# Kernel tuning notes

Hardware: AMD Instinct MI355X
Metric: run time of the kernel (lower is better)

## Reference

```python
import jax, jax.numpy as jnp
import numpy as np

N_NODES = 100000
N_EDGES = 640000
D_IN = 128
D_OUT = 128


def setup_inputs() -> dict:
    key = jax.random.key(0)
    k_x, k_w, k_v, k_r, k_c = jax.random.split(key, 5)
    x = jax.random.normal(k_x, (N_NODES, D_IN), dtype=jnp.float32)
    # Xavier-uniform init for weights, zeros for bias (matches module init)
    limit = float(np.sqrt(6.0 / (D_IN + D_OUT)))
    weights = jax.random.uniform(k_w, (D_IN, D_OUT), dtype=jnp.float32,
                                 minval=-limit, maxval=limit)
    bias = jnp.zeros((D_OUT,), dtype=jnp.float32)
    # Sparse normalized adjacency in COO form: value[e] * y[col[e]] scattered to row[e]
    edge_val = jax.random.uniform(k_v, (N_EDGES,), dtype=jnp.float32)
    row = jax.random.randint(k_r, (N_EDGES,), 0, N_NODES, dtype=jnp.int32)
    col = jax.random.randint(k_c, (N_EDGES,), 0, N_NODES, dtype=jnp.int32)
    return {"x": x, "weights": weights, "bias": bias,
            "edge_val": edge_val, "row": row, "col": col}


def reference(x, weights, bias, edge_val, row, col):
    # y = x @ W  (dense GEMM)  [N, D_OUT]
    y = x @ weights
    # SpMM: out[i] = sum_{e: row[e]==i} edge_val[e] * y[col[e]]
    msg = edge_val[:, None] * y[col]            # [E, D_OUT] irregular gather
    agg = jax.ops.segment_sum(msg, row, num_segments=x.shape[0])
    return agg + bias
```

## Files before the change

### kernel.cpp

```cpp
#include <hip/hip_runtime.h>
#include <hip/hip_bf16.h>


#define N_NODES 100000
#define N_EDGES 640000
#define D 128
#define ELL_K 16
#define OVF_CAP 8192
#define NB 391
#define BCAP 2048
#define CHUNK 4096
#define NCHUNKS 157

typedef __attribute__((ext_vector_type(8))) short short8;
typedef __attribute__((ext_vector_type(4))) float f32x4;
typedef __attribute__((ext_vector_type(4))) ushort us4;

__device__ __forceinline__ ushort f2bf(float f) {
    uint u = __float_as_uint(f);
    u += 0x7fff + ((u >> 16) & 1);
    return (ushort)(u >> 16);
}
__device__ __forceinline__ float bflo(uint u) { return __uint_as_float(u << 16); }
__device__ __forceinline__ float bfhi(uint u) { return __uint_as_float(u & 0xffff0000u); }

__global__ __launch_bounds__(256, 2) void gemm_xw(const float* __restrict__ x,
                                                  const float* __restrict__ w,
                                                  ushort* __restrict__ y,
                                                  int* __restrict__ bucketCursor,
                                                  int* __restrict__ ovfCnt) {
    __shared__ ushort wt[128 * 128];
    const int tid = threadIdx.x;

    int gz = blockIdx.x * 256 + tid;
    if (gz < NB) bucketCursor[gz] = gz * BCAP;
    if (gz == 0) *ovfCnt = 0;

    #pragma unroll
    for (int it = 0; it < 16; ++it) {
        int idx4 = tid + it * 256;
        int k = idx4 >> 5;
        int n0 = (idx4 & 31) * 4;
        float4 v = *(const float4*)(w + (size_t)idx4 * 4);
        float vv[4] = {v.x, v.y, v.z, v.w};
        #pragma unroll
        for (int q = 0; q < 4; ++q) {
            int n = n0 + q;
            wt[n * 128 + (k ^ ((n & 7) << 3))] = f2bf(vv[q]);
        }
    }
    __syncthreads();

    const int lane = tid & 63;
    const int l15 = lane & 15;
    const int h = lane >> 4;

    short8 bfr[8][4];
    #pragma unroll
    for (int j = 0; j < 8; ++j) {
        int n = 16 * j + l15;
        #pragma unroll
        for (int ks = 0; ks < 4; ++ks) {
            int k0 = 32 * ks + 8 * h;
            bfr[j][ks] = *(const short8*)&wt[n * 128 + (k0 ^ ((n & 7) << 3))];
        }
    }

    const int waveGlobal = blockIdx.x * 4 + (tid >> 6);
    const int nWaves = gridDim.x * 4;
    const int nTiles = N_NODES / 16;

    for (int t = waveGlobal; t < nTiles; t += nWaves) {
        const float* xr = x + (size_t)(t * 16 + l15) * D;
        float4 xb[8];
        #pragma unroll
        for (int ks = 0; ks < 4; ++ks) {
            xb[2 * ks]     = *(const float4*)(xr + 32 * ks + 8 * h);
            xb[2 * ks + 1] = *(const float4*)(xr + 32 * ks + 8 * h + 4);
        }
        f32x4 acc[8];
        #pragma unroll
        for (int j = 0; j < 8; ++j) acc[j] = (f32x4){0.f, 0.f, 0.f, 0.f};
        #pragma unroll
        for (int ks = 0; ks < 4; ++ks) {
            const float* p0 = (const float*)&xb[2 * ks];
            const float* p1 = (const float*)&xb[2 * ks + 1];
            short8 a;
            a[0] = f2bf(p0[0]); a[1] = f2bf(p0[1]); a[2] = f2bf(p0[2]); a[3] = f2bf(p0[3]);
            a[4] = f2bf(p1[0]); a[5] = f2bf(p1[1]); a[6] = f2bf(p1[2]); a[7] = f2bf(p1[3]);
            #pragma unroll
            for (int j = 0; j < 8; ++j)
                acc[j] = __builtin_amdgcn_mfma_f32_16x16x32_bf16(bfr[j][ks], a, acc[j], 0, 0, 0);
        }
        ushort* yn = y + (size_t)(t * 16 + l15) * D;
        #pragma unroll
        for (int j = 0; j < 8; ++j) {
            us4 o;
            o.x = f2bf(acc[j][0]); o.y = f2bf(acc[j][1]);
            o.z = f2bf(acc[j][2]); o.w = f2bf(acc[j][3]);
            *(us4*)(yn + 16 * j + 4 * h) = o;
        }
    }
}

__global__ __launch_bounds__(256) void partition_edges(const float* __restrict__ ev,
                                                       const int* __restrict__ row,
                                                       const int* __restrict__ col,
                                                       int* __restrict__ bucketCursor,
                                                       uint2* __restrict__ es0,
                                                       int* __restrict__ ovfCnt,
                                                       int* __restrict__ ovfRow,
                                                       int* __restrict__ ovfCol,
                                                       float* __restrict__ ovfVal) {
    __shared__ int hist[NB];
    __shared__ int cur[NB];
    const int tid = threadIdx.x;
    const int base = blockIdx.x * CHUNK;

    for (int t = tid; t < NB; t += 256) hist[t] = 0;
    __syncthreads();

    #pragma unroll
    for (int it = 0; it < CHUNK / 256; ++it) {
        int i = base + it * 256 + tid;
        if (i < N_EDGES) atomicAdd(&hist[row[i] >> 8], 1);
    }
    __syncthreads();

    for (int t = tid; t < NB; t += 256) {
        int hcnt = hist[t];
        cur[t] = (hcnt > 0) ? atomicAdd(&bucketCursor[t], hcnt) : 0;
    }
    __syncthreads();

    #pragma unroll
    for (int it = 0; it < CHUNK / 256; ++it) {
        int i = base + it * 256 + tid;
        if (i < N_EDGES) {
            int r = row[i];
            int b = r >> 8;
            int p = atomicAdd(&cur[b], 1);
            if (p < (b + 1) * BCAP) {
                uint2 e;
                e.x = __float_as_uint(ev[i]);
                e.y = (uint)col[i] | ((uint)(r & 255) << 20);
                es0[p] = e;
            } else {
                int q = atomicAdd(ovfCnt, 1);
                if (q < OVF_CAP) {
                    ovfRow[q] = r;
                    ovfCol[q] = col[i];
                    ovfVal[q] = ev[i];
                }
            }
        }
    }
}

__global__ __launch_bounds__(256) void build_ell(const uint2* __restrict__ es0,
                                                 const int* __restrict__ bucketCursor,
                                                 float2* __restrict__ es,
                                                 int* __restrict__ counts,
                                                 int* __restrict__ ovfCnt,
                                                 int* __restrict__ ovfRow,
                                                 int* __restrict__ ovfCol,
                                                 float* __restrict__ ovfVal) {
    __shared__ float2 ell[256 * ELL_K];
    __shared__ int lcnt[256];
    const int tid = threadIdx.x;
    const int b = blockIdx.x;

    lcnt[tid] = 0;
    __syncthreads();

    int cnt = bucketCursor[b] - b * BCAP;
    if (cnt > BCAP) cnt = BCAP;
    const uint2* src = es0 + (size_t)b * BCAP;

    for (int i = tid; i < cnt; i += 256) {
        uint2 e = src[i];
        int r = e.y >> 20;
        int p = atomicAdd(&lcnt[r], 1);
        if (p < ELL_K) {
            float2 rec;
            rec.x = __uint_as_float(e.x);
            rec.y = __uint_as_float(e.y & 0xFFFFFu);
            ell[r * ELL_K + p] = rec;
        } else {
            int q = atomicAdd(ovfCnt, 1);
            if (q < OVF_CAP) {
                ovfRow[q] = b * 256 + r;
                ovfCol[q] = (int)(e.y & 0xFFFFFu);
                ovfVal[q] = __uint_as_float(e.x);
            }
        }
    }
    __syncthreads();

    const int nbase = b * 256;
    int nvalid = N_NODES - nbase;
    if (nvalid > 256) nvalid = 256;

    if (tid < nvalid) counts[nbase + tid] = lcnt[tid];

    float4* dst4 = (float4*)(es + (size_t)nbase * ELL_K);
    const float4* ell4 = (const float4*)ell;
    for (int t = tid; t < nvalid * (ELL_K / 2); t += 256)
        dst4[t] = ell4[t];
}

__global__ __launch_bounds__(256) void spmm_ell(const ushort* __restrict__ y,
                                                const float2* __restrict__ es,
                                                const int* __restrict__ counts,
                                                const float* __restrict__ bias,
                                                float* __restrict__ out) {
    const int tid = threadIdx.x;
    const int lane = tid & 63;
    const int wid = blockIdx.x * 4 + (tid >> 6);
    const float2 b2 = *(const float2*)(bias + lane * 2);

    #pragma unroll 1
    for (int rep = 0; rep < 2; ++rep) {
        const int n = __builtin_amdgcn_readfirstlane(wid * 2 + rep);
        int deg = counts[n];
        if (deg > ELL_K) deg = ELL_K;
        const float4* er = (const float4*)(es + (size_t)n * ELL_K);

        float ax = 0.f, ay = 0.f;
        #pragma unroll
        for (int g = 0; g < 4; ++g) {
            if (4 * g < deg) {
                float4 sA = er[2 * g];
                float4 sB = er[2 * g + 1];
                int c0 = __float_as_int(sA.y);
                int c1 = (4 * g + 1 < deg) ? __float_as_int(sA.w) : c0;
                int c2 = (4 * g + 2 < deg) ? __float_as_int(sB.y) : c0;
                int c3 = (4 * g + 3 < deg) ? __float_as_int(sB.w) : c0;
                uint u0 = *(const uint*)(y + ((size_t)c0 << 7) + lane * 2);
                uint u1 = *(const uint*)(y + ((size_t)c1 << 7) + lane * 2);
                uint u2 = *(const uint*)(y + ((size_t)c2 << 7) + lane * 2);
                uint u3 = *(const uint*)(y + ((size_t)c3 << 7) + lane * 2);
                float v0 = sA.x;
                float v1 = (4 * g + 1 < deg) ? sA.z : 0.f;
                float v2 = (4 * g + 2 < deg) ? sB.x : 0.f;
                float v3 = (4 * g + 3 < deg) ? sB.z : 0.f;
                ax += v0 * bflo(u0); ay += v0 * bfhi(u0);
                ax += v1 * bflo(u1); ay += v1 * bfhi(u1);
                ax += v2 * bflo(u2); ay += v2 * bfhi(u2);
                ax += v3 * bflo(u3); ay += v3 * bfhi(u3);
            }
        }
        float2 o = {ax + b2.x, ay + b2.y};
        *(float2*)(out + ((size_t)n << 7) + lane * 2) = o;
    }
}

__global__ void ovf_fix(const ushort* __restrict__ y, const int* __restrict__ ovfRow,
                        const int* __restrict__ ovfCol, const float* __restrict__ ovfVal,
                        const int* __restrict__ ovfCnt, float* __restrict__ out) {
    int nOvf = *ovfCnt;
    if (nOvf > OVF_CAP) nOvf = OVF_CAP;
    int total = nOvf * 32;
    for (int idx = blockIdx.x * 256 + threadIdx.x; idx < total; idx += gridDim.x * 256) {
        int e = idx >> 5;
        int c = idx & 31;
        int r = ovfRow[e];
        int col = ovfCol[e];
        float v = ovfVal[e];
        uint2 u = *(const uint2*)(y + ((size_t)col << 7) + c * 4);
        atomicAdd(&out[(size_t)r * D + c * 4 + 0], v * bflo(u.x));
        atomicAdd(&out[(size_t)r * D + c * 4 + 1], v * bfhi(u.x));
        atomicAdd(&out[(size_t)r * D + c * 4 + 2], v * bflo(u.y));
        atomicAdd(&out[(size_t)r * D + c * 4 + 3], v * bfhi(u.y));
    }
}

extern "C" void kernel_launch(void* const* d_in, const int* in_sizes, int n_in,
                              void* d_out, int out_size, void* d_ws, size_t ws_size,
                              hipStream_t stream) {
    const float* x = (const float*)d_in[0];
    const float* w = (const float*)d_in[1];
    const float* bias = (const float*)d_in[2];
    const float* ev = (const float*)d_in[3];
    const int* row = (const int*)d_in[4];
    const int* col = (const int*)d_in[5];
    float* out = (float*)d_out;

    size_t off = 0;
    auto carve = [&](size_t bytes) -> void* {
        void* p = (char*)d_ws + off;
        off += (bytes + 255) & ~(size_t)255;
        return p;
    };
    ushort* y = (ushort*)carve((size_t)N_NODES * D * sizeof(ushort));
    int* counts = (int*)carve((size_t)N_NODES * sizeof(int));
    float2* es = (float2*)carve((size_t)N_NODES * ELL_K * sizeof(float2));
    uint2* es0 = (uint2*)carve((size_t)NB * BCAP * sizeof(uint2));
    int* bucketCursor = (int*)carve(NB * sizeof(int));
    int* ovfCnt = (int*)carve(sizeof(int));
    int* ovfRow = (int*)carve(OVF_CAP * sizeof(int));
    int* ovfCol = (int*)carve(OVF_CAP * sizeof(int));
    float* ovfVal = (float*)carve(OVF_CAP * sizeof(float));

    gemm_xw<<<512, 256, 0, stream>>>(x, w, y, bucketCursor, ovfCnt);
    partition_edges<<<NCHUNKS, 256, 0, stream>>>(ev, row, col, bucketCursor, es0,
                                                 ovfCnt, ovfRow, ovfCol, ovfVal);
    build_ell<<<NB, 256, 0, stream>>>(es0, bucketCursor, es, counts,
                                      ovfCnt, ovfRow, ovfCol, ovfVal);
    spmm_ell<<<N_NODES / 8, 256, 0, stream>>>(y, es, counts, bias, out);
    ovf_fix<<<16, 256, 0, stream>>>(y, ovfRow, ovfCol, ovfVal, ovfCnt, out);
}
```

Baseline: 85.75 us.

## Fuse GEMM with edge partitioning and widen SpMM gathers to 16-byte loads

Merges the dense GEMM and the edge-partition pass into one launch. The first blocks bucket edges while the remaining blocks compute tiles of the GEMM, so the two independent stages can run concurrently and one launch is removed. Cursor initialisation moves to a memset and bucket counts are now kept relative to each bucket. In the SpMM, each wave now handles four nodes per step with 16 lanes per row and uint4 loads, which widens the gather accesses. This adds more registers per lane, and the memset adds a small extra operation to the stream.

```diff
diff --git a/kernel.cpp b/kernel.cpp
--- a/kernel.cpp
+++ b/kernel.cpp
@@ -11,6 +11,8 @@
 #define BCAP 2048
 #define CHUNK 4096
 #define NCHUNKS 157
+#define GEMM_BLOCKS 782
+#define N_TILES 6250
 
 typedef __attribute__((ext_vector_type(8))) short short8;
 typedef __attribute__((ext_vector_type(4))) float f32x4;
@@ -24,17 +26,69 @@
 __device__ __forceinline__ float bflo(uint u) { return __uint_as_float(u << 16); }
 __device__ __forceinline__ float bfhi(uint u) { return __uint_as_float(u & 0xffff0000u); }
 
-__global__ __launch_bounds__(256, 2) void gemm_xw(const float* __restrict__ x,
-                                                  const float* __restrict__ w,
-                                                  ushort* __restrict__ y,
-                                                  int* __restrict__ bucketCursor,
-                                                  int* __restrict__ ovfCnt) {
-    __shared__ ushort wt[128 * 128];
+__global__ __launch_bounds__(256, 2) void gemm_partition(const float* __restrict__ x,
+                                                         const float* __restrict__ w,
+                                                         ushort* __restrict__ y,
+                                                         const float* __restrict__ ev,
+                                                         const int* __restrict__ row,
+                                                         const int* __restrict__ col,
+                                                         int* __restrict__ bucketCnt,
+                                                         uint2* __restrict__ es0,
+                                                         int* __restrict__ ovfCnt,
+                                                         int* __restrict__ ovfRow,
+                                                         int* __restrict__ ovfCol,
+                                                         float* __restrict__ ovfVal) {
+    __shared__ union {
+        ushort wt[128 * 128];
+        struct { int hist[NB]; int cur[NB]; } p;
+    } sm;
     const int tid = threadIdx.x;
 
-    int gz = blockIdx.x * 256 + tid;
-    if (gz < NB) bucketCursor[gz] = gz * BCAP;
-    if (gz == 0) *ovfCnt = 0;
+    if (blockIdx.x < NCHUNKS) {
+        const int base = blockIdx.x * CHUNK;
+        for (int t = tid; t < NB; t += 256) sm.p.hist[t] = 0;
+        __syncthreads();
+
+        #pragma unroll
+        for (int it = 0; it < CHUNK / 256; ++it) {
+            int i = base + it * 256 + tid;
+            if (i < N_EDGES) atomicAdd(&sm.p.hist[row[i] >> 8], 1);
+        }
+        __syncthreads();
+
+        for (int t = tid; t < NB; t += 256) {
+            int h = sm.p.hist[t];
+            int start = (h > 0) ? atomicAdd(&bucketCnt[t], h) : 0;
+            sm.p.cur[t] = t * BCAP + start;
+        }
+        __syncthreads();
+
+        #pragma unroll
+        for (int it = 0; it < CHUNK / 256; ++it) {
+            int i = base + it * 256 + tid;
+            if (i < N_EDGES) {
+                int r = row[i];
+                int b = r >> 8;
+                int p = atomicAdd(&sm.p.cur[b], 1);
+                if (p < (b + 1) * BCAP) {
+                    uint2 e;
+                    e.x = __float_as_uint(ev[i]);
+                    e.y = (uint)col[i] | ((uint)(r & 255) << 20);
+                    es0[p] = e;
+                } else {
+                    int q = atomicAdd(ovfCnt, 1);
+                    if (q < OVF_CAP) {
+                        ovfRow[q] = r;
+                        ovfCol[q] = col[i];
+                        ovfVal[q] = ev[i];
+                    }
+                }
+            }
+        }
+        return;
+    }
+
+    const int bid = blockIdx.x - NCHUNKS;
 
     #pragma unroll
     for (int it = 0; it < 16; ++it) {
@@ -46,7 +100,7 @@
         #pragma unroll
         for (int q = 0; q < 4; ++q) {
             int n = n0 + q;
-            wt[n * 128 + (k ^ ((n & 7) << 3))] = f2bf(vv[q]);
+            sm.wt[n * 128 + (k ^ ((n & 7) << 3))] = f2bf(vv[q]);
         }
     }
     __syncthreads();
@@ -62,15 +116,15 @@
         #pragma unroll
         for (int ks = 0; ks < 4; ++ks) {
             int k0 = 32 * ks + 8 * h;
-            bfr[j][ks] = *(const short8*)&wt[n * 128 + (k0 ^ ((n & 7) << 3))];
-        }
-    }
-
-    const int waveGlobal = blockIdx.x * 4 + (tid >> 6);
-    const int nWaves = gridDim.x * 4;
-    const int nTiles = N_NODES / 16;
-
-    for (int t = waveGlobal; t < nTiles; t += nWaves) {
+            bfr[j][ks] = *(const short8*)&sm.wt[n * 128 + (k0 ^ ((n & 7) << 3))];
+        }
+    }
+
+    const int t0 = bid * 8 + (tid >> 6) * 2;
+    #pragma unroll 1
+    for (int rep = 0; rep < 2; ++rep) {
+        int t = t0 + rep;
+        if (t >= N_TILES) continue;
         const float* xr = x + (size_t)(t * 16 + l15) * D;
         float4 xb[8];
         #pragma unroll
@@ -103,62 +157,8 @@
     }
 }
 
-__global__ __launch_bounds__(256) void partition_edges(const float* __restrict__ ev,
-                                                       const int* __restrict__ row,
-                                                       const int* __restrict__ col,
-                                                       int* __restrict__ bucketCursor,
-                                                       uint2* __restrict__ es0,
-                                                       int* __restrict__ ovfCnt,
-                                                       int* __restrict__ ovfRow,
-                                                       int* __restrict__ ovfCol,
-                                                       float* __restrict__ ovfVal) {
-    __shared__ int hist[NB];
-    __shared__ int cur[NB];
-    const int tid = threadIdx.x;
-    const int base = blockIdx.x * CHUNK;
-
-    for (int t = tid; t < NB; t += 256) hist[t] = 0;
-    __syncthreads();
-
-    #pragma unroll
-    for (int it = 0; it < CHUNK / 256; ++it) {
-        int i = base + it * 256 + tid;
-        if (i < N_EDGES) atomicAdd(&hist[row[i] >> 8], 1);
-    }
-    __syncthreads();
-
-    for (int t = tid; t < NB; t += 256) {
-        int hcnt = hist[t];
-        cur[t] = (hcnt > 0) ? atomicAdd(&bucketCursor[t], hcnt) : 0;
-    }
-    __syncthreads();
-
-    #pragma unroll
-    for (int it = 0; it < CHUNK / 256; ++it) {
-        int i = base + it * 256 + tid;
-        if (i < N_EDGES) {
-            int r = row[i];
-            int b = r >> 8;
-            int p = atomicAdd(&cur[b], 1);
-            if (p < (b + 1) * BCAP) {
-                uint2 e;
-                e.x = __float_as_uint(ev[i]);
-                e.y = (uint)col[i] | ((uint)(r & 255) << 20);
-                es0[p] = e;
-            } else {
-                int q = atomicAdd(ovfCnt, 1);
-                if (q < OVF_CAP) {
-                    ovfRow[q] = r;
-                    ovfCol[q] = col[i];
-                    ovfVal[q] = ev[i];
-                }
-            }
-        }
-    }
-}
-
 __global__ __launch_bounds__(256) void build_ell(const uint2* __restrict__ es0,
-                                                 const int* __restrict__ bucketCursor,
+                                                 const int* __restrict__ bucketCnt,
                                                  float2* __restrict__ es,
                                                  int* __restrict__ counts,
                                                  int* __restrict__ ovfCnt,
@@ -173,7 +173,7 @@
     lcnt[tid] = 0;
     __syncthreads();
 
-    int cnt = bucketCursor[b] - b * BCAP;
+    int cnt = bucketCnt[b];
     if (cnt > BCAP) cnt = BCAP;
     const uint2* src = es0 + (size_t)b * BCAP;
 
@@ -216,17 +216,23 @@
                                                 float* __restrict__ out) {
     const int tid = threadIdx.x;
     const int lane = tid & 63;
+    const int c16 = lane & 15;
+    const int sub = lane >> 4;
     const int wid = blockIdx.x * 4 + (tid >> 6);
-    const float2 b2 = *(const float2*)(bias + lane * 2);
+
+    const float4 b0 = *(const float4*)(bias + c16 * 8);
+    const float4 b1 = *(const float4*)(bias + c16 * 8 + 4);
 
     #pragma unroll 1
     for (int rep = 0; rep < 2; ++rep) {
-        const int n = __builtin_amdgcn_readfirstlane(wid * 2 + rep);
+        const int n = wid * 8 + rep * 4 + sub;
         int deg = counts[n];
         if (deg > ELL_K) deg = ELL_K;
         const float4* er = (const float4*)(es + (size_t)n * ELL_K);
 
-        float ax = 0.f, ay = 0.f;
+        float a0 = 0.f, a1 = 0.f, a2 = 0.f, a3 = 0.f;
+        float a4 = 0.f, a5 = 0.f, a6 = 0.f, a7 = 0.f;
+
         #pragma unroll
         for (int g = 0; g < 4; ++g) {
             if (4 * g < deg) {
@@ -236,22 +242,37 @@
                 int c1 = (4 * g + 1 < deg) ? __float_as_int(sA.w) : c0;
                 int c2 = (4 * g + 2 < deg) ? __float_as_int(sB.y) : c0;
                 int c3 = (4 * g + 3 < deg) ? __float_as_int(sB.w) : c0;
-                uint u0 = *(const uint*)(y + ((size_t)c0 << 7) + lane * 2);
-                uint u1 = *(const uint*)(y + ((size_t)c1 << 7) + lane * 2);
-                uint u2 = *(const uint*)(y + ((size_t)c2 << 7) + lane * 2);
-                uint u3 = *(const uint*)(y + ((size_t)c3 << 7) + lane * 2);
+                uint4 u0 = *(const uint4*)(y + ((size_t)c0 << 7) + c16 * 8);
+                uint4 u1 = *(const uint4*)(y + ((size_t)c1 << 7) + c16 * 8);
+                uint4 u2 = *(const uint4*)(y + ((size_t)c2 << 7) + c16 * 8);
+                uint4 u3 = *(const uint4*)(y + ((size_t)c3 << 7) + c16 * 8);
                 float v0 = sA.x;
                 float v1 = (4 * g + 1 < deg) ? sA.z : 0.f;
                 float v2 = (4 * g + 2 < deg) ? sB.x : 0.f;
                 float v3 = (4 * g + 3 < deg) ? sB.z : 0.f;
-                ax += v0 * bflo(u0); ay += v0 * bfhi(u0);
-                ax += v1 * bflo(u1); ay += v1 * bfhi(u1);
-                ax += v2 * bflo(u2); ay += v2 * bfhi(u2);
-                ax += v3 * bflo(u3); ay += v3 * bfhi(u3);
+                a0 += v0 * bflo(u0.x); a1 += v0 * bfhi(u0.x);
+                a2 += v0 * bflo(u0.y); a3 += v0 * bfhi(u0.y);
+                a4 += v0 * bflo(u0.z); a5 += v0 * bfhi(u0.z);
+                a6 += v0 * bflo(u0.w); a7 += v0 * bfhi(u0.w);
+                a0 += v1 * bflo(u1.x); a1 += v1 * bfhi(u1.x);
+                a2 += v1 * bflo(u1.y); a3 += v1 * bfhi(u1.y);
+                a4 += v1 * bflo(u1.z); a5 += v1 * bfhi(u1.z);
+                a6 += v1 * bflo(u1.w); a7 += v1 * bfhi(u1.w);
+                a0 += v2 * bflo(u2.x); a1 += v2 * bfhi(u2.x);
+                a2 += v2 * bflo(u2.y); a3 += v2 * bfhi(u2.y);
+                a4 += v2 * bflo(u2.z); a5 += v2 * bfhi(u2.z);
+                a6 += v2 * bflo(u2.w); a7 += v2 * bfhi(u2.w);
+                a0 += v3 * bflo(u3.x); a1 += v3 * bfhi(u3.x);
+                a2 += v3 * bflo(u3.y); a3 += v3 * bfhi(u3.y);
+                a4 += v3 * bflo(u3.z); a5 += v3 * bfhi(u3.z);
+                a6 += v3 * bflo(u3.w); a7 += v3 * bfhi(u3.w);
             }
         }
-        float2 o = {ax + b2.x, ay + b2.y};
-        *(float2*)(out + ((size_t)n << 7) + lane * 2) = o;
+        float4 o0 = {a0 + b0.x, a1 + b0.y, a2 + b0.z, a3 + b0.w};
+        float4 o1 = {a4 + b1.x, a5 + b1.y, a6 + b1.z, a7 + b1.w};
+        float* orow = out + ((size_t)n << 7) + c16 * 8;
+        *(float4*)orow = o0;
+        *(float4*)(orow + 4) = o1;
     }
 }
 
@@ -296,17 +317,18 @@
     int* counts = (int*)carve((size_t)N_NODES * sizeof(int));
     float2* es = (float2*)carve((size_t)N_NODES * ELL_K * sizeof(float2));
     uint2* es0 = (uint2*)carve((size_t)NB * BCAP * sizeof(uint2));
-    int* bucketCursor = (int*)carve(NB * sizeof(int));
-    int* ovfCnt = (int*)carve(sizeof(int));
+    int* bucketCnt = (int*)carve((NB + 1) * sizeof(int));
+    int* ovfCnt = bucketCnt + NB;
     int* ovfRow = (int*)carve(OVF_CAP * sizeof(int));
     int* ovfCol = (int*)carve(OVF_CAP * sizeof(int));
     float* ovfVal = (float*)carve(OVF_CAP * sizeof(float));
 
-    gemm_xw<<<512, 256, 0, stream>>>(x, w, y, bucketCursor, ovfCnt);
-    partition_edges<<<NCHUNKS, 256, 0, stream>>>(ev, row, col, bucketCursor, es0,
-                                                 ovfCnt, ovfRow, ovfCol, ovfVal);
-    build_ell<<<NB, 256, 0, stream>>>(es0, bucketCursor, es, counts,
+    hipMemsetAsync(bucketCnt, 0, (NB + 1) * sizeof(int), stream);
+
+    gemm_partition<<<NCHUNKS + GEMM_BLOCKS, 256, 0, stream>>>(
+        x, w, y, ev, row, col, bucketCnt, es0, ovfCnt, ovfRow, ovfCol, ovfVal);
+    build_ell<<<NB, 256, 0, stream>>>(es0, bucketCnt, es, counts,
                                       ovfCnt, ovfRow, ovfCol, ovfVal);
-    spmm_ell<<<N_NODES / 8, 256, 0, stream>>>(y, es, counts, bias, out);
+    spmm_ell<<<N_NODES / 32, 256, 0, stream>>>(y, es, counts, bias, out);
     ovf_fix<<<16, 256, 0, stream>>>(y, ovfRow, ovfCol, ovfVal, ovfCnt, out);
 }
```

Result: no change. 86.94 us (+1.4%).

## Widen SpMM gathers to 16-byte loads with quarter-wave rows and pad ELL smem

Applied to the files above, without the earlier changes.

The SpMM kernel now assigns each 16-lane quarter-wave to one node, with each lane loading 8 bf16 values (16 bytes) per neighbour row. Each wave handles 8 nodes, interleaving two node streams to raise memory-level parallelism, and the grid shrinks accordingly. The ELL staging buffer in shared memory is padded to stride 17 to reduce bank conflicts. Bucket counters are simplified to zero-based counts, with the overflow counter folded into the same array. Per-thread register pressure grows and the ELL writeback becomes 8-byte instead of 16-byte stores.

```diff
diff --git a/kernel.cpp b/kernel.cpp
--- a/kernel.cpp
+++ b/kernel.cpp
@@ -11,6 +11,7 @@
 #define BCAP 2048
 #define CHUNK 4096
 #define NCHUNKS 157
+#define N_TILES 6250
 
 typedef __attribute__((ext_vector_type(8))) short short8;
 typedef __attribute__((ext_vector_type(4))) float f32x4;
@@ -27,14 +28,12 @@
 __global__ __launch_bounds__(256, 2) void gemm_xw(const float* __restrict__ x,
                                                   const float* __restrict__ w,
                                                   ushort* __restrict__ y,
-                                                  int* __restrict__ bucketCursor,
-                                                  int* __restrict__ ovfCnt) {
+                                                  int* __restrict__ bucketCnt) {
     __shared__ ushort wt[128 * 128];
     const int tid = threadIdx.x;
 
     int gz = blockIdx.x * 256 + tid;
-    if (gz < NB) bucketCursor[gz] = gz * BCAP;
-    if (gz == 0) *ovfCnt = 0;
+    if (gz <= NB) bucketCnt[gz] = 0;
 
     #pragma unroll
     for (int it = 0; it < 16; ++it) {
@@ -68,9 +67,8 @@
 
     const int waveGlobal = blockIdx.x * 4 + (tid >> 6);
     const int nWaves = gridDim.x * 4;
-    const int nTiles = N_NODES / 16;
-
-    for (int t = waveGlobal; t < nTiles; t += nWaves) {
+
+    for (int t = waveGlobal; t < N_TILES; t += nWaves) {
         const float* xr = x + (size_t)(t * 16 + l15) * D;
         float4 xb[8];
         #pragma unroll
@@ -106,7 +104,7 @@
 __global__ __launch_bounds__(256) void partition_edges(const float* __restrict__ ev,
                                                        const int* __restrict__ row,
                                                        const int* __restrict__ col,
-                                                       int* __restrict__ bucketCursor,
+                                                       int* __restrict__ bucketCnt,
                                                        uint2* __restrict__ es0,
                                                        int* __restrict__ ovfCnt,
                                                        int* __restrict__ ovfRow,
@@ -128,8 +126,9 @@
     __syncthreads();
 
     for (int t = tid; t < NB; t += 256) {
-        int hcnt = hist[t];
-        cur[t] = (hcnt > 0) ? atomicAdd(&bucketCursor[t], hcnt) : 0;
+        int h = hist[t];
+        int start = (h > 0) ? atomicAdd(&bucketCnt[t], h) : 0;
+        cur[t] = t * BCAP + start;
     }
     __syncthreads();
 
@@ -157,15 +156,16 @@
     }
 }
 
+#define ELL_P 17
 __global__ __launch_bounds__(256) void build_ell(const uint2* __restrict__ es0,
-                                                 const int* __restrict__ bucketCursor,
+                                                 const int* __restrict__ bucketCnt,
                                                  float2* __restrict__ es,
                                                  int* __restrict__ counts,
                                                  int* __restrict__ ovfCnt,
                                                  int* __restrict__ ovfRow,
                                                  int* __restrict__ ovfCol,
                                                  float* __restrict__ ovfVal) {
-    __shared__ float2 ell[256 * ELL_K];
+    __shared__ float2 ell[256 * ELL_P];
     __shared__ int lcnt[256];
     const int tid = threadIdx.x;
     const int b = blockIdx.x;
@@ -173,7 +173,7 @@
     lcnt[tid] = 0;
     __syncthreads();
 
-    int cnt = bucketCursor[b] - b * BCAP;
+    int cnt = bucketCnt[b];
     if (cnt > BCAP) cnt = BCAP;
     const uint2* src = es0 + (size_t)b * BCAP;
 
@@ -185,7 +185,7 @@
             float2 rec;
             rec.x = __uint_as_float(e.x);
             rec.y = __uint_as_float(e.y & 0xFFFFFu);
-            ell[r * ELL_K + p] = rec;
+            ell[r * ELL_P + p] = rec;
         } else {
             int q = atomicAdd(ovfCnt, 1);
             if (q < OVF_CAP) {
@@ -203,10 +203,11 @@
 
     if (tid < nvalid) counts[nbase + tid] = lcnt[tid];
 
-    float4* dst4 = (float4*)(es + (size_t)nbase * ELL_K);
-    const float4* ell4 = (const float4*)ell;
-    for (int t = tid; t < nvalid * (ELL_K / 2); t += 256)
-        dst4[t] = ell4[t];
+    float2* dst2 = es + (size_t)nbase * ELL_K;
+    for (int t = tid; t < nvalid * ELL_K; t += 256) {
+        int r = t >> 4, s = t & 15;
+        dst2[t] = ell[r * ELL_P + s];
+    }
 }
 
 __global__ __launch_bounds__(256) void spmm_ell(const ushort* __restrict__ y,
@@ -216,43 +217,112 @@
                                                 float* __restrict__ out) {
     const int tid = threadIdx.x;
     const int lane = tid & 63;
+    const int c16 = lane & 15;
+    const int sub = lane >> 4;
     const int wid = blockIdx.x * 4 + (tid >> 6);
-    const float2 b2 = *(const float2*)(bias + lane * 2);
-
-    #pragma unroll 1
-    for (int rep = 0; rep < 2; ++rep) {
-        const int n = __builtin_amdgcn_readfirstlane(wid * 2 + rep);
-        int deg = counts[n];
-        if (deg > ELL_K) deg = ELL_K;
-        const float4* er = (const float4*)(es + (size_t)n * ELL_K);
-
-        float ax = 0.f, ay = 0.f;
-        #pragma unroll
-        for (int g = 0; g < 4; ++g) {
-            if (4 * g < deg) {
-                float4 sA = er[2 * g];
-                float4 sB = er[2 * g + 1];
-                int c0 = __float_as_int(sA.y);
-                int c1 = (4 * g + 1 < deg) ? __float_as_int(sA.w) : c0;
-                int c2 = (4 * g + 2 < deg) ? __float_as_int(sB.y) : c0;
-                int c3 = (4 * g + 3 < deg) ? __float_as_int(sB.w) : c0;
-                uint u0 = *(const uint*)(y + ((size_t)c0 << 7) + lane * 2);
-                uint u1 = *(const uint*)(y + ((size_t)c1 << 7) + lane * 2);
-                uint u2 = *(const uint*)(y + ((size_t)c2 << 7) + lane * 2);
-                uint u3 = *(const uint*)(y + ((size_t)c3 << 7) + lane * 2);
-                float v0 = sA.x;
-                float v1 = (4 * g + 1 < deg) ? sA.z : 0.f;
-                float v2 = (4 * g + 2 < deg) ? sB.x : 0.f;
-                float v3 = (4 * g + 3 < deg) ? sB.z : 0.f;
-                ax += v0 * bflo(u0); ay += v0 * bfhi(u0);
-                ax += v1 * bflo(u1); ay += v1 * bfhi(u1);
-                ax += v2 * bflo(u2); ay += v2 * bfhi(u2);
-                ax += v3 * bflo(u3); ay += v3 * bfhi(u3);
-            }
-        }
-        float2 o = {ax + b2.x, ay + b2.y};
-        *(float2*)(out + ((size_t)n << 7) + lane * 2) = o;
-    }
+
+    const float4 b0 = *(const float4*)(bias + c16 * 8);
+    const float4 b1 = *(const float4*)(bias + c16 * 8 + 4);
+
+    const int nA = wid * 8 + sub;
+    const int nB = nA + 4;
+    int degA = counts[nA]; if (degA > ELL_K) degA = ELL_K;
+    int degB = counts[nB]; if (degB > ELL_K) degB = ELL_K;
+    const float4* erA = (const float4*)(es + (size_t)nA * ELL_K);
+    const float4* erB = (const float4*)(es + (size_t)nB * ELL_K);
+
+    float aA[8] = {0.f, 0.f, 0.f, 0.f, 0.f, 0.f, 0.f, 0.f};
+    float aB[8] = {0.f, 0.f, 0.f, 0.f, 0.f, 0.f, 0.f, 0.f};
+
+    #pragma unroll
+    for (int g = 0; g < 4; ++g) {
+        const bool pA = 4 * g < degA;
+        const bool pB = 4 * g < degB;
+        float4 sA0, sA1, sB0, sB1;
+        uint4 uA0, uA1, uA2, uA3, uB0, uB1, uB2, uB3;
+        float vA0, vA1, vA2, vA3, vB0, vB1, vB2, vB3;
+
+        if (pA) { sA0 = erA[2 * g]; sA1 = erA[2 * g + 1]; }
+        if (pB) { sB0 = erB[2 * g]; sB1 = erB[2 * g + 1]; }
+
+        if (pA) {
+            int c0 = __float_as_int(sA0.y);
+            int c1 = (4 * g + 1 < degA) ? __float_as_int(sA0.w) : c0;
+            int c2 = (4 * g + 2 < degA) ? __float_as_int(sA1.y) : c0;
+            int c3 = (4 * g + 3 < degA) ? __float_as_int(sA1.w) : c0;
+            uA0 = *(const uint4*)(y + ((size_t)c0 << 7) + c16 * 8);
+            uA1 = *(const uint4*)(y + ((size_t)c1 << 7) + c16 * 8);
+            uA2 = *(const uint4*)(y + ((size_t)c2 << 7) + c16 * 8);
+            uA3 = *(const uint4*)(y + ((size_t)c3 << 7) + c16 * 8);
+            vA0 = sA0.x;
+            vA1 = (4 * g + 1 < degA) ? sA0.z : 0.f;
+            vA2 = (4 * g + 2 < degA) ? sA1.x : 0.f;
+            vA3 = (4 * g + 3 < degA) ? sA1.z : 0.f;
+        }
+        if (pB) {
+            int c0 = __float_as_int(sB0.y);
+            int c1 = (4 * g + 1 < degB) ? __float_as_int(sB0.w) : c0;
+            int c2 = (4 * g + 2 < degB) ? __float_as_int(sB1.y) : c0;
+            int c3 = (4 * g + 3 < degB) ? __float_as_int(sB1.w) : c0;
+            uB0 = *(const uint4*)(y + ((size_t)c0 << 7) + c16 * 8);
+            uB1 = *(const uint4*)(y + ((size_t)c1 << 7) + c16 * 8);
+            uB2 = *(const uint4*)(y + ((size_t)c2 << 7) + c16 * 8);
+            uB3 = *(const uint4*)(y + ((size_t)c3 << 7) + c16 * 8);
+            vB0 = sB0.x;
+            vB1 = (4 * g + 1 < degB) ? sB0.z : 0.f;
+            vB2 = (4 * g + 2 < degB) ? sB1.x : 0.f;
+            vB3 = (4 * g + 3 < degB) ? sB1.z : 0.f;
+        }
+
+        if (pA) {
+            aA[0] += vA0 * bflo(uA0.x); aA[1] += vA0 * bfhi(uA0.x);
+            aA[2] += vA0 * bflo(uA0.y); aA[3] += vA0 * bfhi(uA0.y);
+            aA[4] += vA0 * bflo(uA0.z); aA[5] += vA0 * bfhi(uA0.z);
+            aA[6] += vA0 * bflo(uA0.w); aA[7] += vA0 * bfhi(uA0.w);
+            aA[0] += vA1 * bflo(uA1.x); aA[1] += vA1 * bfhi(uA1.x);
+            aA[2] += vA1 * bflo(uA1.y); aA[3] += vA1 * bfhi(uA1.y);
+            aA[4] += vA1 * bflo(uA1.z); aA[5] += vA1 * bfhi(uA1.z);
+            aA[6] += vA1 * bflo(uA1.w); aA[7] += vA1 * bfhi(uA1.w);
+            aA[0] += vA2 * bflo(uA2.x); aA[1] += vA2 * bfhi(uA2.x);
+            aA[2] += vA2 * bflo(uA2.y); aA[3] += vA2 * bfhi(uA2.y);
+            aA[4] += vA2 * bflo(uA2.z); aA[5] += vA2 * bfhi(uA2.z);
+            aA[6] += vA2 * bflo(uA2.w); aA[7] += vA2 * bfhi(uA2.w);
+            aA[0] += vA3 * bflo(uA3.x); aA[1] += vA3 * bfhi(uA3.x);
+            aA[2] += vA3 * bflo(uA3.y); aA[3] += vA3 * bfhi(uA3.y);
+            aA[4] += vA3 * bflo(uA3.z); aA[5] += vA3 * bfhi(uA3.z);
+            aA[6] += vA3 * bflo(uA3.w); aA[7] += vA3 * bfhi(uA3.w);
+        }
+        if (pB) {
+            aB[0] += vB0 * bflo(uB0.x); aB[1] += vB0 * bfhi(uB0.x);
+            aB[2] += vB0 * bflo(uB0.y); aB[3] += vB0 * bfhi(uB0.y);
+            aB[4] += vB0 * bflo(uB0.z); aB[5] += vB0 * bfhi(uB0.z);
+            aB[6] += vB0 * bflo(uB0.w); aB[7] += vB0 * bfhi(uB0.w);
+            aB[0] += vB1 * bflo(uB1.x); aB[1] += vB1 * bfhi(uB1.x);
+            aB[2] += vB1 * bflo(uB1.y); aB[3] += vB1 * bfhi(uB1.y);
+            aB[4] += vB1 * bflo(uB1.z); aB[5] += vB1 * bfhi(uB1.z);
+            aB[6] += vB1 * bflo(uB1.w); aB[7] += vB1 * bfhi(uB1.w);
+            aB[0] += vB2 * bflo(uB2.x); aB[1] += vB2 * bfhi(uB2.x);
+            aB[2] += vB2 * bflo(uB2.y); aB[3] += vB2 * bfhi(uB2.y);
+            aB[4] += vB2 * bflo(uB2.z); aB[5] += vB2 * bfhi(uB2.z);
+            aB[6] += vB2 * bflo(uB2.w); aB[7] += vB2 * bfhi(uB2.w);
+            aB[0] += vB3 * bflo(uB3.x); aB[1] += vB3 * bfhi(uB3.x);
+            aB[2] += vB3 * bflo(uB3.y); aB[3] += vB3 * bfhi(uB3.y);
+            aB[4] += vB3 * bflo(uB3.z); aB[5] += vB3 * bfhi(uB3.z);
+            aB[6] += vB3 * bflo(uB3.w); aB[7] += vB3 * bfhi(uB3.w);
+        }
+    }
+
+    float4 oA0 = {aA[0] + b0.x, aA[1] + b0.y, aA[2] + b0.z, aA[3] + b0.w};
+    float4 oA1 = {aA[4] + b1.x, aA[5] + b1.y, aA[6] + b1.z, aA[7] + b1.w};
+    float* orA = out + ((size_t)nA << 7) + c16 * 8;
+    *(float4*)orA = oA0;
+    *(float4*)(orA + 4) = oA1;
+
+    float4 oB0 = {aB[0] + b0.x, aB[1] + b0.y, aB[2] + b0.z, aB[3] + b0.w};
+    float4 oB1 = {aB[4] + b1.x, aB[5] + b1.y, aB[6] + b1.z, aB[7] + b1.w};
+    float* orB = out + ((size_t)nB << 7) + c16 * 8;
+    *(float4*)orB = oB0;
+    *(float4*)(orB + 4) = oB1;
 }
 
 __global__ void ovf_fix(const ushort* __restrict__ y, const int* __restrict__ ovfRow,
@@ -296,17 +366,17 @@
     int* counts = (int*)carve((size_t)N_NODES * sizeof(int));
     float2* es = (float2*)carve((size_t)N_NODES * ELL_K * sizeof(float2));
     uint2* es0 = (uint2*)carve((size_t)NB * BCAP * sizeof(uint2));
-    int* bucketCursor = (int*)carve(NB * sizeof(int));
-    int* ovfCnt = (int*)carve(sizeof(int));
+    int* bucketCnt = (int*)carve((NB + 1) * sizeof(int));
+    int* ovfCnt = bucketCnt + NB;
     int* ovfRow = (int*)carve(OVF_CAP * sizeof(int));
     int* ovfCol = (int*)carve(OVF_CAP * sizeof(int));
     float* ovfVal = (float*)carve(OVF_CAP * sizeof(float));
 
-    gemm_xw<<<512, 256, 0, stream>>>(x, w, y, bucketCursor, ovfCnt);
-    partition_edges<<<NCHUNKS, 256, 0, stream>>>(ev, row, col, bucketCursor, es0,
+    gemm_xw<<<512, 256, 0, stream>>>(x, w, y, bucketCnt);
+    partition_edges<<<NCHUNKS, 256, 0, stream>>>(ev, row, col, bucketCnt, es0,
                                                  ovfCnt, ovfRow, ovfCol, ovfVal);
-    build_ell<<<NB, 256, 0, stream>>>(es0, bucketCursor, es, counts,
+    build_ell<<<NB, 256, 0, stream>>>(es0, bucketCnt, es, counts,
                                       ovfCnt, ovfRow, ovfCol, ovfVal);
-    spmm_ell<<<N_NODES / 8, 256, 0, stream>>>(y, es, counts, bias, out);
+    spmm_ell<<<N_NODES / 32, 256, 0, stream>>>(y, es, counts, bias, out);
     ovf_fix<<<16, 256, 0, stream>>>(y, ovfRow, ovfCol, ovfVal, ovfCnt, out);
 }
```

New measurement: 90.00 us. 1.05x slower.
